# Kernel tuning notes

Measured on AMD Instinct MI355X. Metric: run time of the kernel, lower is better.

Reference implementation:

```python
import jax, jax.numpy as jnp
from jax import lax
import numpy as np

B, T, H, OUT = 8, 1500, 1280, 4096
MAXTOK = 375
N_INNER = 3  # 1 mandatory integrate-and-fire iteration + 2 gated extras (alpha<1 => 1 suffices)


def _forward_cif(hidden, alphas, num_tokens, max_tok):
    # hidden: [B, T, D], alphas: [B, T], num_tokens: [B] int32
    Bv, Tv, _ = hidden.shape
    nm1 = num_tokens - 1
    bidx = jnp.arange(Bv)

    def step(carry, xs):
        integrate, token_index = carry  # [B] float, [B] int32
        alpha_t, not_last = xs
        col = jnp.zeros((Bv, max_tok), alphas.dtype)
        alpha = alpha_t
        alpha_needed = 1.0 - integrate
        integrate = integrate + alpha
        ready = integrate >= 1.0
        remainds = jnp.zeros_like(alpha)
        active = jnp.any(ready) | True  # first body iteration always runs (do-while)
        active = jnp.asarray(True)
        for _ in range(N_INNER):
            n_int = jnp.where(ready, integrate - 1.0, integrate)
            a_int = jnp.where(ready, alpha_needed, alpha)
            n_col = col.at[bidx, token_index].set(a_int)
            n_rem = alpha - a_int
            n_tok = jnp.minimum(token_index + ready.astype(token_index.dtype), nm1)
            n_ready = n_int >= 1.0
            integrate = jnp.where(active, n_int, integrate)
            col = jnp.where(active, n_col, col)
            remainds = jnp.where(active, n_rem, remainds)
            token_index = jnp.where(active, n_tok, token_index)
            alpha = jnp.where(active, n_rem, alpha)
            alpha_needed = jnp.where(active, jnp.ones_like(alpha_needed), alpha_needed)
            ready = jnp.where(active, n_ready, jnp.zeros_like(ready))
            active = active & jnp.any(ready)
        # torch adds remainds into column t at step t+1 (so last column never gets it)
        col = jnp.where(not_last, col.at[bidx, token_index].add(remainds), col)
        return (integrate, token_index), col

    init = (jnp.zeros((Bv,), alphas.dtype), jnp.zeros((Bv,), jnp.int32))
    xs = (alphas.T, jnp.arange(Tv) < Tv - 1)  # per-step alpha column, not-last flag
    _, cols = lax.scan(step, init, xs)  # cols: [T, B, max_tok]
    weights = jnp.transpose(cols, (1, 2, 0))  # [B, max_tok, T]
    return jnp.einsum('bmt,btd->bmd', weights, hidden)


def setup_inputs() -> dict:
    key = jax.random.key(0)
    ks = jax.random.split(key, 4)
    audio_features = jax.random.normal(ks[0], (B, T, H), jnp.float32)
    num_tokens = jax.random.randint(ks[1], (B,), 100, MAXTOK + 1).astype(jnp.int32)
    rms_w = jnp.ones((H,), jnp.float32) * 0.4
    cif_w = jax.random.normal(ks[2], (H - 1, H), jnp.float32) / np.sqrt(H - 1)
    cif_b = jnp.zeros((H,), jnp.float32)
    text_w = jax.random.normal(ks[3], (H, OUT), jnp.float32) / np.sqrt(H)
    text_b = jnp.zeros((OUT,), jnp.float32)
    return dict(audio_features=audio_features, num_tokens=num_tokens, rms_w=rms_w,
                cif_w=cif_w, cif_b=cif_b, text_w=text_w, text_b=text_b, max_tokens=MAXTOK)


def reference(audio_features, num_tokens, rms_w, cif_w, cif_b, text_w, text_b, max_tokens):
    alphas = jax.nn.sigmoid(audio_features[:, :, -1])  # [B, T]
    pred_num_tokens = alphas.sum(-1)  # [B]
    alphas = alphas * (num_tokens.astype(alphas.dtype) / pred_num_tokens)[:, None]
    h = _forward_cif(audio_features[:, :, :-1], alphas, num_tokens, max_tokens)  # [B, M, H-1]
    h = h @ cif_w + cif_b  # cif_proj -> [B, M, H]
    d = h.shape[-1]
    rms = jnp.sqrt(jnp.sum(h * h, axis=-1, keepdims=True) / d + 1e-6)
    h = h / rms * rms_w  # RMSNorm(post_ln)
    h = h @ text_w + text_b  # text_proj -> [B, M, OUT]
    return h, pred_num_tokens
```

## Files before the change

### kernel.cpp

```cpp
#include <hip/hip_runtime.h>
#include <hip/hip_bf16.h>
#include <stdint.h>

#define B_ 8
#define T_ 1500
#define H_ 1280
#define HM1 1279
#define OUT_ 4096
#define MTOK 375
#define MROWS (B_*MTOK)
#define KPAD 1280

typedef __attribute__((ext_vector_type(8))) short bf16x8;
typedef __attribute__((ext_vector_type(4))) float f32x4;
typedef unsigned short u16;

static __device__ __forceinline__ u16 f2bf(float f) {
    unsigned int x = __float_as_uint(f);
    unsigned int r = (x + 0x7fffu + ((x >> 16) & 1u)) >> 16;
    return (u16)r;
}
static __device__ __forceinline__ void glds16(const u16* g, u16* l) {
    __builtin_amdgcn_global_load_lds(
        (const __attribute__((address_space(1))) void*)g,
        (__attribute__((address_space(3))) void*)l, 16, 0, 0);
}

__global__ __launch_bounds__(256) void k_front(
    const float* __restrict__ audio, const int* __restrict__ num_tokens,
    const float* __restrict__ rms_w,
    float* __restrict__ pred_out,
    int* __restrict__ tok0, float* __restrict__ w0a,
    int* __restrict__ tok1, float* __restrict__ w1a,
    int* __restrict__ lo, int* __restrict__ hi,
    float* __restrict__ h_sumsq,
    const float* __restrict__ cif_w, const float* __restrict__ text_w,
    u16* __restrict__ cwt, u16* __restrict__ twt)
{
    __shared__ float smem[3514];
    const int tid = threadIdx.x;

    if (blockIdx.x < B_) {
        const int b = blockIdx.x;
        float* al = smem;
        float* ip = smem + 1500;
        float* red = smem + 3000;
        int*   redI = (int*)(smem + 3256);
        float* scale_sh = smem + 3512;

        float sig[6];
        float s = 0.f;
        #pragma unroll
        for (int i = 0; i < 6; ++i) {
            int t = tid + i*256;
            sig[i] = 0.f;
            if (t < T_) {
                float x = audio[((size_t)b*T_ + t)*H_ + (H_-1)];
                sig[i] = 1.f / (1.f + expf(-x));
                s += sig[i];
            }
        }
        red[tid] = s; __syncthreads();
        for (int off = 128; off > 0; off >>= 1) {
            if (tid < off) red[tid] += red[tid+off];
            __syncthreads();
        }
        if (tid == 0) {
            float pred = red[0];
            pred_out[b] = pred;
            *scale_sh = (float)num_tokens[b] / pred;
        }
        __syncthreads();
        float scale = *scale_sh;
        #pragma unroll
        for (int i = 0; i < 6; ++i) {
            int t = tid + i*256;
            if (t < T_) al[t] = sig[i] * scale;
        }
        for (int m = tid; m < MTOK; m += 256) {
            lo[b*MTOK+m] = T_; hi[b*MTOK+m] = 0;
            h_sumsq[b*MTOK+m] = 0.f;
        }
        if (tid == 0) lo[b*MTOK] = 0;
        __syncthreads();

        if (tid == 0) {
            float integ = 0.f;
            float4 cur = *(const float4*)&al[0];
            for (int t = 0; t < T_; t += 4) {
                float4 nxt = (t + 4 < T_) ? *(const float4*)&al[t+4]
                                          : make_float4(0.f,0.f,0.f,0.f);
                float av[4] = {cur.x, cur.y, cur.z, cur.w};
                float ipv[4];
                #pragma unroll
                for (int j = 0; j < 4; ++j) {
                    ipv[j] = integ;
                    float sx = integ + av[j];
                    integ = (sx >= 1.f) ? (sx - 1.f) : sx;
                }
                *(float4*)&ip[t] = *(float4*)ipv;
                cur = nxt;
            }
        }
        __syncthreads();

        const int t0 = tid * 6;
        const int nm1 = num_tokens[b] - 1;
        int fires[6];
        int cnt = 0;
        if (t0 < T_) {
            #pragma unroll
            for (int j = 0; j < 6; ++j) {
                int t = t0 + j;
                float sx = ip[t] + al[t];
                fires[j] = (sx >= 1.f) ? 1 : 0;
                cnt += fires[j];
            }
        }
        redI[tid] = cnt; __syncthreads();
        #pragma unroll
        for (int off = 1; off < 256; off <<= 1) {
            int v = redI[tid];
            if (tid >= off) v += redI[tid - off];
            __syncthreads();
            redI[tid] = v;
            __syncthreads();
        }
        if (t0 < T_) {
            int F = redI[tid] - cnt;
            const int base = b*T_;
            #pragma unroll
            for (int j = 0; j < 6; ++j) {
                int t = t0 + j;
                float a = al[t], ipv = ip[t];
                int fire = fires[j];
                F += fire;
                int tk1 = min(F, nm1);
                int tk0 = min(F - fire, nm1);
                float w0 = fire ? (1.f - ipv) : a;
                float w1 = (t < T_-1) ? (a - w0) : 0.f;
                tok0[base+t] = tk0;  w0a[base+t] = w0;
                tok1[base+t] = tk1;  w1a[base+t] = w1;
                if (tk1 != tk0) {
                    hi[b*MTOK + tk0] = t + 1;
                    lo[b*MTOK + tk1] = t;
                }
                if (t == T_-1) hi[b*MTOK + tk1] = T_;
            }
        }
    } else {
        float (*tile)[33] = (float(*)[33])smem;
        int blk = blockIdx.x - B_;
        const float* src; u16* dst; int R, C, bx, by; bool scaled;
        if (blk < 1600) { src = cif_w;  dst = cwt; R = HM1; C = H_;   bx = blk % 40;  by = blk / 40;  scaled = false; }
        else { blk -= 1600; src = text_w; dst = twt; R = H_;  C = OUT_; bx = blk % 128; by = blk / 128; scaled = true; }
        int c0 = bx * 32, r0 = by * 32;
        int lx = tid & 31, ly = tid >> 5;
        #pragma unroll
        for (int j = 0; j < 4; ++j) {
            int r = r0 + ly + j*8;
            tile[ly + j*8][lx] = (r < R) ? src[(size_t)r*C + c0 + lx] : 0.f;
        }
        __syncthreads();
        float rw = scaled ? rms_w[r0 + lx] : 1.f;
        #pragma unroll
        for (int j = 0; j < 4; ++j) {
            int c = c0 + ly + j*8;
            dst[(size_t)c*KPAD + r0 + lx] = f2bf(tile[lx][ly + j*8] * rw);
        }
    }
}

__global__ __launch_bounds__(256) void k3_pool(
    const float* __restrict__ audio,
    const int* __restrict__ tok0, const float* __restrict__ w0a,
    const int* __restrict__ tok1, const float* __restrict__ w1a,
    const int* __restrict__ lo, const int* __restrict__ hi,
    u16* __restrict__ h1b)
{
    __shared__ float wl[1536];
    const int bm = blockIdx.x;
    const int b = bm / MTOK, m = bm % MTOK;
    const int l = lo[bm], h = hi[bm];
    const int tid = threadIdx.x;
    const int len = h - l;

    for (int j = tid; j < len; j += 256) {
        int i0 = b*T_ + l + j;
        float w = 0.f;
        if (tok0[i0] == m) w += w0a[i0];
        if (tok1[i0] == m) w += w1a[i0];
        wl[j] = w;
    }
    __syncthreads();

    const int d4 = tid * 4;
    const int d1 = 1024 + tid;
    const float* rowp = audio + (size_t)(b*T_ + l) * H_;
    float4 acc4 = make_float4(0.f, 0.f, 0.f, 0.f);
    float acc1 = 0.f;
    #pragma unroll 4
    for (int j = 0; j < len; ++j) {
        float w = wl[j];
        const float* row = rowp + (size_t)j * H_;
        float4 r4 = *(const float4*)(row + d4);
        float r1 = (d1 < HM1) ? row[d1] : 0.f;
        acc4.x += w * r4.x; acc4.y += w * r4.y;
        acc4.z += w * r4.z; acc4.w += w * r4.w;
        acc1 += w * r1;
    }
    u16* dst = h1b + (size_t)bm * KPAD;
    ushort4 o;
    o.x = f2bf(acc4.x); o.y = f2bf(acc4.y); o.z = f2bf(acc4.z); o.w = f2bf(acc4.w);
    *(ushort4*)&dst[d4] = o;
    dst[d1] = (d1 < HM1) ? f2bf(acc1) : (u16)0;
}

template<int TM, bool CIF>
__global__ __launch_bounds__(256, 3) void mfma_gemm_bt(
    const u16* __restrict__ A, const u16* __restrict__ Bt,
    const float* __restrict__ bias, void* __restrict__ Cv,
    float* __restrict__ h_sumsq, int M, int N)
{
    constexpr int K = KPAD;
    constexpr int RA = TM / 64;
    constexpr int MI = 4;
    constexpr int NI = (TM == 128) ? 4 : 2;
    __shared__ u16 sA[TM*32];
    __shared__ u16 sB[128*32];
    const int tid = threadIdx.x;
    const int m0 = blockIdx.y * TM, n0 = blockIdx.x * 128;
    const int wave = tid >> 6, lane = tid & 63;
    const int wm = (TM == 128) ? (wave & 1) * 64 : 0;
    const int wn = (TM == 128) ? (wave >> 1) * 64 : wave * 32;
    const int lrow = lane & 15, quad = lane >> 4;

    const int r0 = tid >> 2, sl = tid & 3;
    const int q0 = sl ^ (r0 & 3) ^ ((r0 >> 2) & 3);
    const u16* Ag[RA];
    #pragma unroll
    for (int p = 0; p < RA; ++p)
        Ag[p] = A + (size_t)min(m0 + r0 + 64*p, M - 1) * K + q0 * 8;
    const u16* Bg[2];
    #pragma unroll
    for (int p = 0; p < 2; ++p)
        Bg[p] = Bt + (size_t)(n0 + r0 + 64*p) * K + q0 * 8;

    int offA[MI], offB[NI];
    #pragma unroll
    for (int i = 0; i < MI; ++i) {
        int m = wm + i*16 + lrow;
        offA[i] = m*32 + (quad ^ (m & 3) ^ ((m >> 2) & 3)) * 8;
    }
    #pragma unroll
    for (int i = 0; i < NI; ++i) {
        int n = wn + i*16 + lrow;
        offB[i] = n*32 + (quad ^ (n & 3) ^ ((n >> 2) & 3)) * 8;
    }

    f32x4 acc[MI][NI] = {};

    for (int k0 = 0; k0 < K; k0 += 32) {
        #pragma unroll
        for (int p = 0; p < RA; ++p) glds16(Ag[p] + k0, sA + (tid + 256*p)*8);
        #pragma unroll
        for (int p = 0; p < 2;  ++p) glds16(Bg[p] + k0, sB + (tid + 256*p)*8);
        __syncthreads();
        bf16x8 af[MI], bfr[NI];
        #pragma unroll
        for (int i = 0; i < MI; ++i) af[i]  = *(const bf16x8*)&sA[offA[i]];
        #pragma unroll
        for (int i = 0; i < NI; ++i) bfr[i] = *(const bf16x8*)&sB[offB[i]];
        #pragma unroll
        for (int mi = 0; mi < MI; ++mi)
            #pragma unroll
            for (int ni = 0; ni < NI; ++ni)
                acc[mi][ni] = __builtin_amdgcn_mfma_f32_16x16x32_bf16(
                    af[mi], bfr[ni], acc[mi][ni], 0, 0, 0);
        __syncthreads();
    }

    float bv[NI];
    #pragma unroll
    for (int ni = 0; ni < NI; ++ni) bv[ni] = bias[n0 + wn + ni*16 + lrow];

    #pragma unroll
    for (int mi = 0; mi < MI; ++mi) {
        #pragma unroll
        for (int r = 0; r < 4; ++r) {
            int row = m0 + wm + mi*16 + quad*4 + r;
            if (CIF) {
                float ss = 0.f;
                #pragma unroll
                for (int ni = 0; ni < NI; ++ni) {
                    float v = acc[mi][ni][r] + bv[ni];
                    ss += v * v;
                    if (row < M)
                        ((u16*)Cv)[(size_t)row*N + (n0 + wn + ni*16 + lrow)] = f2bf(v);
                }
                ss += __shfl_xor(ss, 1);
                ss += __shfl_xor(ss, 2);
                ss += __shfl_xor(ss, 4);
                ss += __shfl_xor(ss, 8);
                if (lrow == 0 && row < M) atomicAdd(&h_sumsq[row], ss);
            } else {
                float inv = 1.f;
                if (row < M)
                    inv = 1.f / sqrtf(h_sumsq[row] / (float)H_ + 1e-6f);
                #pragma unroll
                for (int ni = 0; ni < NI; ++ni) {
                    if (row < M)
                        ((float*)Cv)[(size_t)row*N + (n0 + wn + ni*16 + lrow)] =
                            acc[mi][ni][r] * inv + bv[ni];
                }
            }
        }
    }
}

extern "C" void kernel_launch(void* const* d_in, const int* in_sizes, int n_in,
                              void* d_out, int out_size, void* d_ws, size_t ws_size,
                              hipStream_t stream) {
    (void)in_sizes; (void)n_in; (void)out_size; (void)ws_size;
    const float* audio      = (const float*)d_in[0];
    const int*   num_tokens = (const int*)d_in[1];
    const float* rms_w      = (const float*)d_in[2];
    const float* cif_w      = (const float*)d_in[3];
    const float* cif_b      = (const float*)d_in[4];
    const float* text_w     = (const float*)d_in[5];
    const float* text_b     = (const float*)d_in[6];

    float* out  = (float*)d_out;
    float* pred = out + (size_t)MROWS * OUT_;

    char* ws = (char*)d_ws;
    float* h_sumsq = (float*)(ws + 0);
    float* w0a  = (float*)(ws + 48000);
    float* w1a  = (float*)(ws + 96000);
    int*   tok0 = (int*)  (ws + 144000);
    int*   tok1 = (int*)  (ws + 192000);
    int*   lo   = (int*)  (ws + 240000);
    int*   hi   = (int*)  (ws + 252000);
    u16* h1b = (u16*)(ws + 264192);
    u16* cwt = (u16*)(ws + 7944192);
    u16* twt = (u16*)(ws + 11220992);
    u16* hX  = (u16*)(ws + 21706752);

    k_front<<<B_ + 1600 + 5120, 256, 0, stream>>>(
        audio, num_tokens, rms_w, pred, tok0, w0a, tok1, w1a, lo, hi,
        h_sumsq, cif_w, text_w, cwt, twt);
    k3_pool<<<MROWS, 256, 0, stream>>>(audio, tok0, w0a, tok1, w1a, lo, hi, h1b);
    mfma_gemm_bt<64, true><<<dim3(H_/128, (MROWS+63)/64), 256, 0, stream>>>(
        h1b, cwt, cif_b, hX, h_sumsq, MROWS, H_);
    mfma_gemm_bt<128, false><<<dim3(OUT_/128, (MROWS+127)/128), 256, 0, stream>>>(
        hX, twt, text_b, out, h_sumsq, MROWS, OUT_);
}
```

Measured before the change: 249.4 us.

## Triple-buffer GEMM LDS loads and speed up serial CIF integrate scan

The bf16 MFMA GEMM goes from one LDS buffer with two barriers per k-step to a three-stage ring buffer. Global-to-LDS loads are issued two tiles ahead, using explicit vmcnt waits, a single barrier per step and raised wave priority around the MFMAs, so memory latency can overlap compute. The single-thread CIF prefix scan now processes 16 elements per iteration over a zero-padded array and replaces the compare-select with sx - floor(sx). This shortens the serial chain but could differ slightly when alpha sums reach 2 or more, and the GEMM tripling raises LDS use, which may reduce occupancy.

```diff
diff --git a/kernel.cpp b/kernel.cpp
--- a/kernel.cpp
+++ b/kernel.cpp
@@ -4,6 +4,7 @@
 
 #define B_ 8
 #define T_ 1500
+#define TPAD 1504
 #define H_ 1280
 #define HM1 1279
 #define OUT_ 4096
@@ -37,16 +38,16 @@
     const float* __restrict__ cif_w, const float* __restrict__ text_w,
     u16* __restrict__ cwt, u16* __restrict__ twt)
 {
-    __shared__ float smem[3514];
+    __shared__ float smem[3524];
     const int tid = threadIdx.x;
 
     if (blockIdx.x < B_) {
         const int b = blockIdx.x;
         float* al = smem;
-        float* ip = smem + 1500;
-        float* red = smem + 3000;
-        int*   redI = (int*)(smem + 3256);
-        float* scale_sh = smem + 3512;
+        float* ip = smem + TPAD;
+        float* red = smem + 2*TPAD;
+        int*   redI = (int*)(smem + 2*TPAD + 256);
+        float* scale_sh = smem + 2*TPAD + 512;
 
         float sig[6];
         float s = 0.f;
@@ -77,6 +78,7 @@
             int t = tid + i*256;
             if (t < T_) al[t] = sig[i] * scale;
         }
+        if (tid < TPAD - T_) al[T_ + tid] = 0.f;
         for (int m = tid; m < MTOK; m += 256) {
             lo[b*MTOK+m] = T_; hi[b*MTOK+m] = 0;
             h_sumsq[b*MTOK+m] = 0.f;
@@ -86,20 +88,41 @@
 
         if (tid == 0) {
             float integ = 0.f;
-            float4 cur = *(const float4*)&al[0];
-            for (int t = 0; t < T_; t += 4) {
-                float4 nxt = (t + 4 < T_) ? *(const float4*)&al[t+4]
-                                          : make_float4(0.f,0.f,0.f,0.f);
-                float av[4] = {cur.x, cur.y, cur.z, cur.w};
-                float ipv[4];
-                #pragma unroll
-                for (int j = 0; j < 4; ++j) {
-                    ipv[j] = integ;
-                    float sx = integ + av[j];
-                    integ = (sx >= 1.f) ? (sx - 1.f) : sx;
+            float4 c0 = *(const float4*)&al[0];
+            float4 c1 = *(const float4*)&al[4];
+            float4 c2 = *(const float4*)&al[8];
+            float4 c3 = *(const float4*)&al[12];
+            for (int t = 0; t < TPAD; t += 16) {
+                float4 n0, n1, n2, n3;
+                if (t + 16 < TPAD) {
+                    n0 = *(const float4*)&al[t+16];
+                    n1 = *(const float4*)&al[t+20];
+                    n2 = *(const float4*)&al[t+24];
+                    n3 = *(const float4*)&al[t+28];
                 }
-                *(float4*)&ip[t] = *(float4*)ipv;
-                cur = nxt;
+                float4 o0, o1, o2, o3;
+                float sx;
+                o0.x = integ; sx = integ + c0.x; integ = sx - floorf(sx);
+                o0.y = integ; sx = integ + c0.y; integ = sx - floorf(sx);
+                o0.z = integ; sx = integ + c0.z; integ = sx - floorf(sx);
+                o0.w = integ; sx = integ + c0.w; integ = sx - floorf(sx);
+                o1.x = integ; sx = integ + c1.x; integ = sx - floorf(sx);
+                o1.y = integ; sx = integ + c1.y; integ = sx - floorf(sx);
+                o1.z = integ; sx = integ + c1.z; integ = sx - floorf(sx);
+                o1.w = integ; sx = integ + c1.w; integ = sx - floorf(sx);
+                o2.x = integ; sx = integ + c2.x; integ = sx - floorf(sx);
+                o2.y = integ; sx = integ + c2.y; integ = sx - floorf(sx);
+                o2.z = integ; sx = integ + c2.z; integ = sx - floorf(sx);
+                o2.w = integ; sx = integ + c2.w; integ = sx - floorf(sx);
+                o3.x = integ; sx = integ + c3.x; integ = sx - floorf(sx);
+                o3.y = integ; sx = integ + c3.y; integ = sx - floorf(sx);
+                o3.z = integ; sx = integ + c3.z; integ = sx - floorf(sx);
+                o3.w = integ; sx = integ + c3.w; integ = sx - floorf(sx);
+                *(float4*)&ip[t+0]  = o0;
+                *(float4*)&ip[t+4]  = o1;
+                *(float4*)&ip[t+8]  = o2;
+                *(float4*)&ip[t+12] = o3;
+                c0 = n0; c1 = n1; c2 = n2; c3 = n3;
             }
         }
         __syncthreads();
@@ -216,6 +239,8 @@
     dst[d1] = (d1 < HM1) ? f2bf(acc1) : (u16)0;
 }
 
+#define WAITVM(N) asm volatile("s_waitcnt vmcnt(" #N ")" ::: "memory")
+
 template<int TM, bool CIF>
 __global__ __launch_bounds__(256, 3) void mfma_gemm_bt(
     const u16* __restrict__ A, const u16* __restrict__ Bt,
@@ -223,11 +248,12 @@
     float* __restrict__ h_sumsq, int M, int N)
 {
     constexpr int K = KPAD;
+    constexpr int NT = K / 32;
     constexpr int RA = TM / 64;
     constexpr int MI = 4;
     constexpr int NI = (TM == 128) ? 4 : 2;
-    __shared__ u16 sA[TM*32];
-    __shared__ u16 sB[128*32];
+    __shared__ u16 sA[3][TM*32];
+    __shared__ u16 sB[3][128*32];
     const int tid = threadIdx.x;
     const int m0 = blockIdx.y * TM, n0 = blockIdx.x * 128;
     const int wave = tid >> 6, lane = tid & 63;
@@ -258,26 +284,59 @@
         offB[i] = n*32 + (quad ^ (n & 3) ^ ((n >> 2) & 3)) * 8;
     }
 
+    u16 *Ac = sA[0], *An = sA[1], *Af = sA[2];
+    u16 *Bc = sB[0], *Bn = sB[1], *Bf = sB[2];
+
+    auto stage = [&](int kk, u16* da, u16* db) {
+        #pragma unroll
+        for (int p = 0; p < RA; ++p) glds16(Ag[p] + kk, da + (tid + 256*p)*8);
+        #pragma unroll
+        for (int p = 0; p < 2;  ++p) glds16(Bg[p] + kk, db + (tid + 256*p)*8);
+    };
+
     f32x4 acc[MI][NI] = {};
 
-    for (int k0 = 0; k0 < K; k0 += 32) {
-        #pragma unroll
-        for (int p = 0; p < RA; ++p) glds16(Ag[p] + k0, sA + (tid + 256*p)*8);
-        #pragma unroll
-        for (int p = 0; p < 2;  ++p) glds16(Bg[p] + k0, sB + (tid + 256*p)*8);
-        __syncthreads();
+    stage(0,  Ac, Bc);
+    stage(32, An, Bn);
+
+    for (int t = 0; t < NT - 1; ++t) {
+        if constexpr (TM == 128) WAITVM(4); else WAITVM(3);
+        __builtin_amdgcn_s_barrier();
+        asm volatile("" ::: "memory");
+        if (t + 2 < NT) stage((t + 2) * 32, Af, Bf);
         bf16x8 af[MI], bfr[NI];
         #pragma unroll
-        for (int i = 0; i < MI; ++i) af[i]  = *(const bf16x8*)&sA[offA[i]];
-        #pragma unroll
-        for (int i = 0; i < NI; ++i) bfr[i] = *(const bf16x8*)&sB[offB[i]];
+        for (int i = 0; i < MI; ++i) af[i]  = *(const bf16x8*)&Ac[offA[i]];
+        #pragma unroll
+        for (int i = 0; i < NI; ++i) bfr[i] = *(const bf16x8*)&Bc[offB[i]];
+        __builtin_amdgcn_s_setprio(1);
         #pragma unroll
         for (int mi = 0; mi < MI; ++mi)
             #pragma unroll
             for (int ni = 0; ni < NI; ++ni)
                 acc[mi][ni] = __builtin_amdgcn_mfma_f32_16x16x32_bf16(
                     af[mi], bfr[ni], acc[mi][ni], 0, 0, 0);
-        __syncthreads();
+        __builtin_amdgcn_s_setprio(0);
+        u16* ta = Ac; Ac = An; An = Af; Af = ta;
+        u16* tb = Bc; Bc = Bn; Bn = Bf; Bf = tb;
+    }
+    {
+        WAITVM(0);
+        __builtin_amdgcn_s_barrier();
+        asm volatile("" ::: "memory");
+        bf16x8 af[MI], bfr[NI];
+        #pragma unroll
+        for (int i = 0; i < MI; ++i) af[i]  = *(const bf16x8*)&Ac[offA[i]];
+        #pragma unroll
+        for (int i = 0; i < NI; ++i) bfr[i] = *(const bf16x8*)&Bc[offB[i]];
+        __builtin_amdgcn_s_setprio(1);
+        #pragma unroll
+        for (int mi = 0; mi < MI; ++mi)
+            #pragma unroll
+            for (int ni = 0; ni < NI; ++ni)
+                acc[mi][ni] = __builtin_amdgcn_mfma_f32_16x16x32_bf16(
+                    af[mi], bfr[ni], acc[mi][ni], 0, 0, 0);
+        __builtin_amdgcn_s_setprio(0);
     }
 
     float bv[NI];
```

Measured after the change: 237.5 us. 1.05x faster.
